# Optimization experiments

Hardware: AMD Instinct MI355X
Metric: run time of the kernel (lower is better)

The kernel has to match this reference:

```python
import jax, jax.numpy as jnp
import numpy as np

N_HIDDEN = 512

def _lstm_cell(x, h, c, W_ih, W_hh, b):
    # PyTorch LSTMCell: gates ordered i, f, g, o
    gates = x @ W_ih.T + h @ W_hh.T + b  # [B, 4H]
    i, f, g, o = jnp.split(gates, 4, axis=-1)
    i = jax.nn.sigmoid(i)
    f = jax.nn.sigmoid(f)
    g = jnp.tanh(g)
    o = jax.nn.sigmoid(o)
    c_new = f * c + i * g
    h_new = o * jnp.tanh(c_new)
    return h_new, c_new

def setup_inputs() -> dict:
    key = jax.random.key(0)
    ks = jax.random.split(key, 10)
    B, T, H = 256, 1024, N_HIDDEN
    s1 = 1.0 / np.sqrt(H)
    inp = {
        'x': jax.random.normal(ks[0], (B, T), dtype=jnp.float32),
        'W_ih1': jax.random.uniform(ks[1], (4 * H, 1), jnp.float32, -s1, s1),
        'W_hh1': jax.random.uniform(ks[2], (4 * H, H), jnp.float32, -s1, s1),
        'b1': jax.random.uniform(ks[3], (4 * H,), jnp.float32, -s1, s1),
        'W_ih2': jax.random.uniform(ks[4], (4 * H, H), jnp.float32, -s1, s1),
        'W_hh2': jax.random.uniform(ks[5], (4 * H, H), jnp.float32, -s1, s1),
        'b2': jax.random.uniform(ks[6], (4 * H,), jnp.float32, -s1, s1),
        'W_lin': jax.random.uniform(ks[7], (1, H), jnp.float32, -s1, s1),
        'b_lin': jax.random.uniform(ks[8], (1,), jnp.float32, -s1, s1),
    }
    return inp

def reference(x, W_ih1, W_hh1, b1, W_ih2, W_hh2, b2, W_lin, b_lin):
    B, T = x.shape
    H = W_hh1.shape[1]
    zeros = jnp.zeros((B, H), dtype=x.dtype)
    init = (zeros, zeros, zeros, zeros)
    xs = x.T[:, :, None]  # [T, B, 1]

    def step(carry, x_t):
        h1, c1, h2, c2 = carry
        h1, c1 = _lstm_cell(x_t, h1, c1, W_ih1, W_hh1, b1)
        h2, c2 = _lstm_cell(h1, h2, c2, W_ih2, W_hh2, b2)
        out = h2 @ W_lin.T + b_lin  # [B, 1]
        return (h1, c1, h2, c2), out

    _, outs = jax.lax.scan(step, init, xs)  # outs: [T, B, 1]
    return outs[:, :, 0].T  # [B, T]
```

## Files before the change

### kernel.cpp

```cpp
#include <hip/hip_runtime.h>
#include <math.h>

#define BB   256
#define TT   1024
#define HH   512
#define NWG  256
#define NTHR 512
#define SLOT (HH*BB)
#define NSLOT 8
#define PADX 20

typedef _Float16 f16;
typedef _Float16 f16x8 __attribute__((ext_vector_type(8)));
typedef float    f32x4 __attribute__((ext_vector_type(4)));
typedef unsigned int u32;
typedef u32 u32x2 __attribute__((ext_vector_type(2)));
typedef u32 u32x4 __attribute__((ext_vector_type(4)));
typedef unsigned short u16;
typedef unsigned char u8;

__device__ __forceinline__ f32x4 mf(f16x8 a, f16x8 b, f32x4 c){
  return __builtin_amdgcn_mfma_f32_16x16x32_f16(a, b, c, 0, 0, 0);
}

__device__ __forceinline__ float fast_sigmoid(float v){
  float e = __expf(-v);
  return __builtin_amdgcn_rcpf(1.0f + e);
}
__device__ __forceinline__ float fast_tanh(float v){
  float a = fabsf(v);
  float e = __expf(-2.0f * a);
  float r = (1.0f - e) * __builtin_amdgcn_rcpf(1.0f + e);
  return copysignf(r, v);
}

__device__ __forceinline__ void split_h(float hv, u16& hb, u8& lb){
  const f16 hh = (f16)hv;
  const f16 lh = (f16)((hv - (float)hh) * 2048.0f);
  union {f16 f; u16 u;} ch, cl; ch.f = hh; cl.f = lh;
  hb = ch.u;
  lb = (u8)(((u32)cl.u + 0x80u) >> 8);
}
__device__ __forceinline__ float join_h(u16 hb, u8 lb){
  union {u16 u; f16 f;} h, l;
  h.u = hb; l.u = (u16)((u32)lb << 8);
  return (float)h.f + (float)l.f * (1.0f/2048.0f);
}
__device__ __forceinline__ void st_wt_u16(u16* p, u16 v){
  __hip_atomic_store(p, v, __ATOMIC_RELAXED, __HIP_MEMORY_SCOPE_AGENT);
}
__device__ __forceinline__ void st_wt_u8(u8* p, u8 v){
  __hip_atomic_store(p, v, __ATOMIC_RELAXED, __HIP_MEMORY_SCOPE_AGENT);
}
__device__ __forceinline__ void st_wt_f32(float* p, float v){
  __hip_atomic_store(p, v, __ATOMIC_RELAXED, __HIP_MEMORY_SCOPE_AGENT);
}

__device__ __forceinline__ void build2(u32x4 hd, u32x2 ld2, f16x8& fh, f16x8& fl){
  union {u32 u[4]; f16x8 f;} H, L;
  H.u[0]=hd[0]; H.u[1]=hd[1]; H.u[2]=hd[2]; H.u[3]=hd[3];
  L.u[0] = __builtin_amdgcn_perm(ld2[0], 0u, 0x05010400u);
  L.u[1] = __builtin_amdgcn_perm(ld2[0], 0u, 0x07010600u);
  L.u[2] = __builtin_amdgcn_perm(ld2[1], 0u, 0x05010400u);
  L.u[3] = __builtin_amdgcn_perm(ld2[1], 0u, 0x07010600u);
  fh = H.f; fl = L.f;
}

struct St { u32x4 h1h4; u32x2 h1l2; u32x4 h2h4; u32x2 h2l2; };

__device__ __forceinline__ void gridbar_g(unsigned* barb, unsigned ph){
  __syncthreads();
  if (threadIdx.x == 0){
    __builtin_amdgcn_fence(__ATOMIC_RELEASE, "agent");
    const unsigned g = blockIdx.x & 31u;
    unsigned old = __hip_atomic_fetch_add(&barb[g*16], 1u, __ATOMIC_RELAXED, __HIP_MEMORY_SCOPE_AGENT);
    if (old + 1u == 8u*ph){
      unsigned om = __hip_atomic_fetch_add(&barb[512], 1u, __ATOMIC_RELAXED, __HIP_MEMORY_SCOPE_AGENT);
      if (om + 1u == 32u*ph){
        #pragma unroll
        for (int r = 0; r < 32; ++r)
          __hip_atomic_store(&barb[544 + r*16], ph, __ATOMIC_RELAXED, __HIP_MEMORY_SCOPE_AGENT);
      }
    }
    while (__hip_atomic_load(&barb[544 + g*16], __ATOMIC_RELAXED, __HIP_MEMORY_SCOPE_AGENT) < ph){
      __builtin_amdgcn_s_sleep(2);
    }
    __builtin_amdgcn_fence(__ATOMIC_ACQUIRE, "agent");
  }
  __syncthreads();
}

__global__ __launch_bounds__(NTHR, 2) void lstm_mfma(
    const float* __restrict__ x,      const float* __restrict__ W_ih1,
    const float* __restrict__ W_hh1,  const float* __restrict__ b1,
    const float* __restrict__ W_ih2,  const float* __restrict__ W_hh2,
    const float* __restrict__ b2,     const float* __restrict__ W_lin,
    const float* __restrict__ b_lin,  float* __restrict__ out,
    char* __restrict__ wsb)
{
  __shared__ f16x8 A2hi[2048], A2lo[2048], A1hi[1024], A1lo[1024];
  __shared__ float xch[8][16*PADX];
  __shared__ float wlin_s[512];
  __shared__ float outpart[2][8];

  unsigned* bar = (unsigned*)wsb;
  float* xT = (float*)(wsb + 16384);
  u16* h1h = (u16*)(wsb + 16384 + 1048576);
  u8*  h1l = (u8*) ((char*)h1h + 2*NSLOT*SLOT);
  u16* h2h = (u16*)((char*)h1l + NSLOT*SLOT);
  u8*  h2l = (u8*) ((char*)h2h + 2*NSLOT*SLOT);

  const int w   = blockIdx.x,  tid = threadIdx.x;
  const int l   = tid & 63,    wv  = tid >> 6;
  const int quad = l >> 4,     lc  = l & 15;
  const int p = w >> 1, cb = w & 1;
  const int j0 = 4*p;
  const int bcol = cb*128 + wv*16 + lc;
  const int jq = j0 + quad;
  const int b_out = cb*128 + p;
  unsigned* dbar = bar + cb*1024;
  unsigned* gbar = bar + 2048;
  const unsigned grp = (unsigned)(p >> 3);
  const int qrot = p & 3;
  const int hoff = (p>>1)*2048 + bcol*8 + (p&1)*4 + quad;

  {
    const int g_ = lc >> 2, jj_ = lc & 3;
    const int wrow = g_*HH + j0 + jj_;
    const float* rowI  = W_ih2 + (size_t)wrow*HH;
    const float* rowH2 = W_hh2 + (size_t)wrow*HH;
    const float* rowH1 = W_hh1 + (size_t)wrow*HH;
    for (int c = wv; c < 32; c += 8){
      const int kb = c*32 + quad*8;
      union {f16x8 v; f16 e[8];} hi8, lo8;
      #pragma unroll
      for (int i = 0; i < 8; ++i){
        const int k = kb + i;
        const float wval = (k < HH) ? rowI[k] : rowH2[k - HH];
        const f16 h_ = (f16)wval;
        hi8.e[i] = h_;
        lo8.e[i] = (f16)((wval - (float)h_) * 2048.0f);
      }
      A2hi[c*64 + l] = hi8.v;
      A2lo[c*64 + l] = lo8.v;
    }
    for (int c = wv; c < 16; c += 8){
      const int kb = c*32 + quad*8;
      union {f16x8 v; f16 e[8];} hi8, lo8;
      #pragma unroll
      for (int i = 0; i < 8; ++i){
        const float wval = rowH1[kb + i];
        const f16 h_ = (f16)wval;
        hi8.e[i] = h_;
        lo8.e[i] = (f16)((wval - (float)h_) * 2048.0f);
      }
      A1hi[c*64 + l] = hi8.v;
      A1lo[c*64 + l] = lo8.v;
    }
  }
  float wih1r[4], b1r[4], b2r[4];
  #pragma unroll
  for (int g = 0; g < 4; ++g){
    wih1r[g] = W_ih1[g*HH + jq];
    b1r[g]   = b1[g*HH + jq];
    b2r[g]   = b2[g*HH + jq];
  }
  const float blin = b_lin[0];
  wlin_s[tid] = W_lin[tid];

  {
    const int gid = w*NTHR + tid;
    #pragma unroll
    for (int i2 = 0; i2 < 2; ++i2){
      const int idx = gid + i2*131072;
      const int bb2 = idx >> 10, tt2 = idx & (TT-1);
      xT[(size_t)tt2*BB + bb2] = x[idx];
    }
  }
  {
    const int idx = w*NTHR + tid;
    st_wt_u16(&h2h[(NSLOT-1)*SLOT + idx], (u16)0);
    st_wt_u8 (&h2l[(NSLOT-1)*SLOT + idx], (u8)0);
  }

  gridbar_g(gbar, 1);

  float c1, c2 = 0.0f;
  {
    const float xv0 = xT[bcol];
    const float gi = fast_sigmoid(fmaf(xv0, wih1r[0], b1r[0]));
    const float gg = fast_tanh   (fmaf(xv0, wih1r[2], b1r[2]));
    const float go = fast_sigmoid(fmaf(xv0, wih1r[3], b1r[3]));
    c1 = gi * gg;
    const float hv = go * fast_tanh(c1);
    u16 hb; u8 lb; split_h(hv, hb, lb);
    st_wt_u16(&h1h[hoff], hb);
    st_wt_u8 (&h1l[hoff], lb);
  }
  gridbar_g(gbar, 2);

  auto poll_mask = [&](unsigned need) -> unsigned {
    unsigned cv = __hip_atomic_load(&dbar[(l & 15) * 16], __ATOMIC_RELAXED, __HIP_MEMORY_SCOPE_AGENT);
    return (unsigned)__ballot(cv >= need) & 0xFFFFu;
  };

  unsigned got = 0xFFFFu;

  for (int t = 0; t < TT; ++t){
    const int sR1 = ( t            & (NSLOT-1))*SLOT;
    const int sR2 = ((t+NSLOT-1)   & (NSLOT-1))*SLOT;
    const int sW1 = ((t+1)         & (NSLOT-1))*SLOT;
    const int sW2 = ( t            & (NSLOT-1))*SLOT;
    const unsigned need = 8u * (unsigned)t;

    f32x4 aA2 = {0,0,0,0}, aB2 = {0,0,0,0}, aA1 = {0,0,0,0}, aB1 = {0,0,0,0};
    const u16* q1h = h1h + sR1 + quad*2048 + bcol*8;
    const u8*  q1l = h1l + sR1 + quad*2048 + bcol*8;
    const u16* q2h = h2h + sR2 + quad*2048 + bcol*8;
    const u8*  q2l = h2l + sR2 + quad*2048 + bcol*8;

    auto waitq = [&](int qq){
      const unsigned qm = 0xFu << (4*qq);
      while ((got & qm) != qm){
        __builtin_amdgcn_s_sleep(1);
        got |= poll_mask(need);
      }
      asm volatile("" ::: "memory");
    };
    auto ldc = [&](int c) -> St {
      St s;
      s.h1h4 = *(const u32x4*)(q1h + c*8192);
      s.h1l2 = *(const u32x2*)(q1l + c*8192);
      s.h2h4 = *(const u32x4*)(q2h + c*8192);
      s.h2l2 = *(const u32x2*)(q2l + c*8192);
      return s;
    };
    auto cmp = [&](const St& s, int c){
      f16x8 bh, bl;
      build2(s.h1h4, s.h1l2, bh, bl);
      const f16x8 a2h = A2hi[c*64 + l];
      const f16x8 a2l = A2lo[c*64 + l];
      const f16x8 a1h = A1hi[c*64 + l];
      const f16x8 a1l = A1lo[c*64 + l];
      aA2 = mf(a2h, bh, aA2);
      aB2 = mf(a2h, bl, aB2);
      aB2 = mf(a2l, bh, aB2);
      aA1 = mf(a1h, bh, aA1);
      aB1 = mf(a1h, bl, aB1);
      aB1 = mf(a1l, bh, aB1);
      f16x8 ch, cl2;
      build2(s.h2h4, s.h2l2, ch, cl2);
      const f16x8 d2h = A2hi[(c+16)*64 + l];
      const f16x8 d2l = A2lo[(c+16)*64 + l];
      aA2 = mf(d2h, ch, aA2);
      aB2 = mf(d2h, cl2, aB2);
      aB2 = mf(d2l, ch, aB2);
    };

    const int cq0 = 4*qrot;
    const int cq1 = 4*((qrot+1)&3);
    const int cq2 = 4*((qrot+2)&3);
    const int cq3 = 4*((qrot+3)&3);
    St SA0,SA1,SA2,SA3, SB0,SB1,SB2,SB3;
    waitq(cq0 >> 2);
    SA0=ldc(cq0+0); SA1=ldc(cq0+1); SA2=ldc(cq0+2); SA3=ldc(cq0+3);
    waitq(cq1 >> 2);
    SB0=ldc(cq1+0); SB1=ldc(cq1+1); SB2=ldc(cq1+2); SB3=ldc(cq1+3);
    cmp(SA0,cq0+0); cmp(SA1,cq0+1); cmp(SA2,cq0+2); cmp(SA3,cq0+3);
    waitq(cq2 >> 2);
    SA0=ldc(cq2+0); SA1=ldc(cq2+1); SA2=ldc(cq2+2); SA3=ldc(cq2+3);
    cmp(SB0,cq1+0); cmp(SB1,cq1+1); cmp(SB2,cq1+2); cmp(SB3,cq1+3);
    waitq(cq3 >> 2);
    SB0=ldc(cq3+0); SB1=ldc(cq3+1); SB2=ldc(cq3+2); SB3=ldc(cq3+3);
    cmp(SA0,cq2+0); cmp(SA1,cq2+1); cmp(SA2,cq2+2); cmp(SA3,cq2+3);
    cmp(SB0,cq3+0); cmp(SB1,cq3+1); cmp(SB2,cq3+2); cmp(SB3,cq3+3);

    const int oidx = sR2 + (tid>>3)*2048 + b_out*8 + (tid&7);
    float opart = join_h(h2h[oidx], h2l[oidx]) * wlin_s[tid];

    float* xw = &xch[wv][0];
    {
      f32x4 pre;
      #pragma unroll
      for (int i = 0; i < 4; ++i) pre[i] = fmaf(aB2[i], 1.0f/2048.0f, aA2[i]);
      *(f32x4*)&xw[lc*PADX + quad*4] = pre;
      __threadfence_block();
      const float g0 = xw[lc*PADX + 0*4 + quad];
      const float g1 = xw[lc*PADX + 1*4 + quad];
      const float g2 = xw[lc*PADX + 2*4 + quad];
      const float g3 = xw[lc*PADX + 3*4 + quad];
      const float gi = fast_sigmoid(g0 + b2r[0]);
      const float gf = fast_sigmoid(g1 + b2r[1]);
      const float gg = fast_tanh   (g2 + b2r[2]);
      const float go = fast_sigmoid(g3 + b2r[3]);
      c2 = fmaf(gf, c2, gi*gg);
      const float hv = go * fast_tanh(c2);
      u16 hb; u8 lb; split_h(hv, hb, lb);
      st_wt_u16(&h2h[sW2 + hoff], hb);
      st_wt_u8 (&h2l[sW2 + hoff], lb);
    }
    {
      f32x4 pre;
      #pragma unroll
      for (int i = 0; i < 4; ++i) pre[i] = fmaf(aB1[i], 1.0f/2048.0f, aA1[i]);
      __threadfence_block();
      *(f32x4*)&xw[lc*PADX + quad*4] = pre;
      __threadfence_block();
      const float g0 = xw[lc*PADX + 0*4 + quad];
      const float g1 = xw[lc*PADX + 1*4 + quad];
      const float g2 = xw[lc*PADX + 2*4 + quad];
      const float g3 = xw[lc*PADX + 3*4 + quad];
      const int tx = (t+1 < TT) ? (t+1) : (TT-1);
      const float xv = xT[(size_t)tx*BB + bcol];
      const float gi = fast_sigmoid(g0 + fmaf(xv, wih1r[0], b1r[0]));
      const float gf = fast_sigmoid(g1 + fmaf(xv, wih1r[1], b1r[1]));
      const float gg = fast_tanh   (g2 + fmaf(xv, wih1r[2], b1r[2]));
      const float go = fast_sigmoid(g3 + fmaf(xv, wih1r[3], b1r[3]));
      c1 = fmaf(gf, c1, gi*gg);
      const float hv = go * fast_tanh(c1);
      u16 hb; u8 lb; split_h(hv, hb, lb);
      st_wt_u16(&h1h[sW1 + hoff], hb);
      st_wt_u8 (&h1l[sW1 + hoff], lb);
    }
    #pragma unroll
    for (int off = 32; off > 0; off >>= 1) opart += __shfl_down(opart, off, 64);
    if (l == 0) outpart[t & 1][wv] = opart;

    __syncthreads();
    if (tid == 0){
      __builtin_amdgcn_fence(__ATOMIC_RELEASE, "workgroup");
      __hip_atomic_fetch_add(&dbar[grp*16], 1u, __ATOMIC_RELAXED, __HIP_MEMORY_SCOPE_AGENT);
      if (t % 7 == 6){
        __builtin_amdgcn_fence(__ATOMIC_ACQUIRE, "agent");
      }
      if (t > 0){
        float s = blin;
        #pragma unroll
        for (int q2i = 0; q2i < 8; ++q2i) s += outpart[t & 1][q2i];
        st_wt_f32(&out[(size_t)b_out*TT + (t-1)], s);
      }
    }
    got = poll_mask(8u * (unsigned)(t+1));
    __syncthreads();
  }

  {
    const unsigned needT = 8u * (unsigned)TT;
    while (got != 0xFFFFu){
      __builtin_amdgcn_s_sleep(1);
      got |= poll_mask(needT);
    }
    asm volatile("" ::: "memory");

    const int oidx = ((TT-1)&(NSLOT-1))*SLOT + (tid>>3)*2048 + b_out*8 + (tid&7);
    float opart = join_h(h2h[oidx], h2l[oidx]) * wlin_s[tid];
    #pragma unroll
    for (int off = 32; off > 0; off >>= 1) opart += __shfl_down(opart, off, 64);
    if (l == 0) outpart[0][wv] = opart;
    __syncthreads();
    if (tid == 0){
      float s = blin;
      #pragma unroll
      for (int q2i = 0; q2i < 8; ++q2i) s += outpart[0][q2i];
      st_wt_f32(&out[(size_t)b_out*TT + (TT-1)], s);
    }
  }
}

extern "C" void kernel_launch(void* const* d_in, const int* in_sizes, int n_in,
                              void* d_out, int out_size, void* d_ws, size_t ws_size,
                              hipStream_t stream) {
  const float* x     = (const float*)d_in[0];
  const float* W_ih1 = (const float*)d_in[1];
  const float* W_hh1 = (const float*)d_in[2];
  const float* b1    = (const float*)d_in[3];
  const float* W_ih2 = (const float*)d_in[4];
  const float* W_hh2 = (const float*)d_in[5];
  const float* b2    = (const float*)d_in[6];
  const float* W_lin = (const float*)d_in[7];
  const float* b_lin = (const float*)d_in[8];
  float* out = (float*)d_out;
  char* wsb  = (char*)d_ws;

  hipMemsetAsync(d_ws, 0, 16384, stream);

  hipLaunchKernelGGL(lstm_mfma, dim3(NWG), dim3(NTHR), 0, stream,
                     x, W_ih1, W_hh1, b1, W_ih2, W_hh2, b2, W_lin, b_lin, out, wsb);
}
```

Measured before the change: 10.73 ms.

## Split per-step sync into separate h1 and h2 barriers to overlap layers

Each timestep now runs in two phases. First the kernel computes the h1-dependent products and the layer-1 update, then signals a separate h1 counter. Only after that does it wait on h2 chunks for the recurrent layer-2 term. Separate dbar counters, polled with a 32-bit ballot, let layer-1 progress be published earlier so other workgroups can start the next step sooner. The cost is an extra __syncthreads and atomic per step, plus more polling.

```diff
diff --git a/kernel.cpp b/kernel.cpp
--- a/kernel.cpp
+++ b/kernel.cpp
@@ -66,7 +66,7 @@
   fh = H.f; fl = L.f;
 }
 
-struct St { u32x4 h1h4; u32x2 h1l2; u32x4 h2h4; u32x2 h2l2; };
+struct St1 { u32x4 h4; u32x2 l2; };
 
 __device__ __forceinline__ void gridbar_g(unsigned* barb, unsigned ph){
   __syncthreads();
@@ -199,12 +199,14 @@
   }
   gridbar_g(gbar, 2);
 
-  auto poll_mask = [&](unsigned need) -> unsigned {
-    unsigned cv = __hip_atomic_load(&dbar[(l & 15) * 16], __ATOMIC_RELAXED, __HIP_MEMORY_SCOPE_AGENT);
-    return (unsigned)__ballot(cv >= need) & 0xFFFFu;
+  auto poll2 = [&](unsigned need) -> unsigned {
+    const int li = l & 31;
+    const unsigned off = (unsigned)((li & 15) * 16) + ((li & 16) ? 576u : 0u);
+    unsigned cv = __hip_atomic_load(&dbar[off], __ATOMIC_RELAXED, __HIP_MEMORY_SCOPE_AGENT);
+    return (unsigned)__ballot(cv >= need);
   };
 
-  unsigned got = 0xFFFFu;
+  unsigned got = 0xFFFFFFFFu;
 
   for (int t = 0; t < TT; ++t){
     const int sR1 = ( t            & (NSLOT-1))*SLOT;
@@ -219,25 +221,23 @@
     const u16* q2h = h2h + sR2 + quad*2048 + bcol*8;
     const u8*  q2l = h2l + sR2 + quad*2048 + bcol*8;
 
-    auto waitq = [&](int qq){
-      const unsigned qm = 0xFu << (4*qq);
+    auto waitq = [&](int qq, int base){
+      const unsigned qm = 0xFu << (base + 4*qq);
       while ((got & qm) != qm){
         __builtin_amdgcn_s_sleep(1);
-        got |= poll_mask(need);
+        got |= poll2(need);
       }
       asm volatile("" ::: "memory");
     };
-    auto ldc = [&](int c) -> St {
-      St s;
-      s.h1h4 = *(const u32x4*)(q1h + c*8192);
-      s.h1l2 = *(const u32x2*)(q1l + c*8192);
-      s.h2h4 = *(const u32x4*)(q2h + c*8192);
-      s.h2l2 = *(const u32x2*)(q2l + c*8192);
-      return s;
+    auto ldc1 = [&](int c) -> St1 {
+      St1 s; s.h4 = *(const u32x4*)(q1h + c*8192); s.l2 = *(const u32x2*)(q1l + c*8192); return s;
     };
-    auto cmp = [&](const St& s, int c){
+    auto ldc2 = [&](int c) -> St1 {
+      St1 s; s.h4 = *(const u32x4*)(q2h + c*8192); s.l2 = *(const u32x2*)(q2l + c*8192); return s;
+    };
+    auto cmp1 = [&](const St1& s, int c){
       f16x8 bh, bl;
-      build2(s.h1h4, s.h1l2, bh, bl);
+      build2(s.h4, s.l2, bh, bl);
       const f16x8 a2h = A2hi[c*64 + l];
       const f16x8 a2l = A2lo[c*64 + l];
       const f16x8 a1h = A1hi[c*64 + l];
@@ -248,8 +248,10 @@
       aA1 = mf(a1h, bh, aA1);
       aB1 = mf(a1h, bl, aB1);
       aB1 = mf(a1l, bh, aB1);
+    };
+    auto cmp2 = [&](const St1& s, int c){
       f16x8 ch, cl2;
-      build2(s.h2h4, s.h2l2, ch, cl2);
+      build2(s.h4, s.l2, ch, cl2);
       const f16x8 d2h = A2hi[(c+16)*64 + l];
       const f16x8 d2l = A2lo[(c+16)*64 + l];
       aA2 = mf(d2h, ch, aA2);
@@ -261,44 +263,24 @@
     const int cq1 = 4*((qrot+1)&3);
     const int cq2 = 4*((qrot+2)&3);
     const int cq3 = 4*((qrot+3)&3);
-    St SA0,SA1,SA2,SA3, SB0,SB1,SB2,SB3;
-    waitq(cq0 >> 2);
-    SA0=ldc(cq0+0); SA1=ldc(cq0+1); SA2=ldc(cq0+2); SA3=ldc(cq0+3);
-    waitq(cq1 >> 2);
-    SB0=ldc(cq1+0); SB1=ldc(cq1+1); SB2=ldc(cq1+2); SB3=ldc(cq1+3);
-    cmp(SA0,cq0+0); cmp(SA1,cq0+1); cmp(SA2,cq0+2); cmp(SA3,cq0+3);
-    waitq(cq2 >> 2);
-    SA0=ldc(cq2+0); SA1=ldc(cq2+1); SA2=ldc(cq2+2); SA3=ldc(cq2+3);
-    cmp(SB0,cq1+0); cmp(SB1,cq1+1); cmp(SB2,cq1+2); cmp(SB3,cq1+3);
-    waitq(cq3 >> 2);
-    SB0=ldc(cq3+0); SB1=ldc(cq3+1); SB2=ldc(cq3+2); SB3=ldc(cq3+3);
-    cmp(SA0,cq2+0); cmp(SA1,cq2+1); cmp(SA2,cq2+2); cmp(SA3,cq2+3);
-    cmp(SB0,cq3+0); cmp(SB1,cq3+1); cmp(SB2,cq3+2); cmp(SB3,cq3+3);
-
-    const int oidx = sR2 + (tid>>3)*2048 + b_out*8 + (tid&7);
-    float opart = join_h(h2h[oidx], h2l[oidx]) * wlin_s[tid];
+
+    {
+      St1 SA0,SA1,SA2,SA3, SB0,SB1,SB2,SB3;
+      waitq(cq0 >> 2, 16);
+      SA0=ldc1(cq0+0); SA1=ldc1(cq0+1); SA2=ldc1(cq0+2); SA3=ldc1(cq0+3);
+      waitq(cq1 >> 2, 16);
+      SB0=ldc1(cq1+0); SB1=ldc1(cq1+1); SB2=ldc1(cq1+2); SB3=ldc1(cq1+3);
+      cmp1(SA0,cq0+0); cmp1(SA1,cq0+1); cmp1(SA2,cq0+2); cmp1(SA3,cq0+3);
+      waitq(cq2 >> 2, 16);
+      SA0=ldc1(cq2+0); SA1=ldc1(cq2+1); SA2=ldc1(cq2+2); SA3=ldc1(cq2+3);
+      cmp1(SB0,cq1+0); cmp1(SB1,cq1+1); cmp1(SB2,cq1+2); cmp1(SB3,cq1+3);
+      waitq(cq3 >> 2, 16);
+      SB0=ldc1(cq3+0); SB1=ldc1(cq3+1); SB2=ldc1(cq3+2); SB3=ldc1(cq3+3);
+      cmp1(SA0,cq2+0); cmp1(SA1,cq2+1); cmp1(SA2,cq2+2); cmp1(SA3,cq2+3);
+      cmp1(SB0,cq3+0); cmp1(SB1,cq3+1); cmp1(SB2,cq3+2); cmp1(SB3,cq3+3);
+    }
 
     float* xw = &xch[wv][0];
-    {
-      f32x4 pre;
-      #pragma unroll
-      for (int i = 0; i < 4; ++i) pre[i] = fmaf(aB2[i], 1.0f/2048.0f, aA2[i]);
-      *(f32x4*)&xw[lc*PADX + quad*4] = pre;
-      __threadfence_block();
-      const float g0 = xw[lc*PADX + 0*4 + quad];
-      const float g1 = xw[lc*PADX + 1*4 + quad];
-      const float g2 = xw[lc*PADX + 2*4 + quad];
-      const float g3 = xw[lc*PADX + 3*4 + quad];
-      const float gi = fast_sigmoid(g0 + b2r[0]);
-      const float gf = fast_sigmoid(g1 + b2r[1]);
-      const float gg = fast_tanh   (g2 + b2r[2]);
-      const float go = fast_sigmoid(g3 + b2r[3]);
-      c2 = fmaf(gf, c2, gi*gg);
-      const float hv = go * fast_tanh(c2);
-      u16 hb; u8 lb; split_h(hv, hb, lb);
-      st_wt_u16(&h2h[sW2 + hoff], hb);
-      st_wt_u8 (&h2l[sW2 + hoff], lb);
-    }
     {
       f32x4 pre;
       #pragma unroll
@@ -322,6 +304,55 @@
       st_wt_u16(&h1h[sW1 + hoff], hb);
       st_wt_u8 (&h1l[sW1 + hoff], lb);
     }
+    __syncthreads();
+    if (tid == 0){
+      __builtin_amdgcn_fence(__ATOMIC_RELEASE, "workgroup");
+      __hip_atomic_fetch_add(&dbar[576 + grp*16], 1u, __ATOMIC_RELAXED, __HIP_MEMORY_SCOPE_AGENT);
+    }
+
+    u16 ohb; u8 olb;
+    {
+      St1 SA0,SA1,SA2,SA3, SB0,SB1,SB2,SB3;
+      waitq(cq0 >> 2, 0);
+      SA0=ldc2(cq0+0); SA1=ldc2(cq0+1); SA2=ldc2(cq0+2); SA3=ldc2(cq0+3);
+      waitq(cq1 >> 2, 0);
+      SB0=ldc2(cq1+0); SB1=ldc2(cq1+1); SB2=ldc2(cq1+2); SB3=ldc2(cq1+3);
+      cmp2(SA0,cq0+0); cmp2(SA1,cq0+1); cmp2(SA2,cq0+2); cmp2(SA3,cq0+3);
+      waitq(cq2 >> 2, 0);
+      SA0=ldc2(cq2+0); SA1=ldc2(cq2+1); SA2=ldc2(cq2+2); SA3=ldc2(cq2+3);
+      cmp2(SB0,cq1+0); cmp2(SB1,cq1+1); cmp2(SB2,cq1+2); cmp2(SB3,cq1+3);
+      waitq(cq3 >> 2, 0);
+      SB0=ldc2(cq3+0); SB1=ldc2(cq3+1); SB2=ldc2(cq3+2); SB3=ldc2(cq3+3);
+      const int oidx = sR2 + (tid>>3)*2048 + b_out*8 + (tid&7);
+      ohb = h2h[oidx];
+      olb = h2l[oidx];
+      cmp2(SA0,cq2+0); cmp2(SA1,cq2+1); cmp2(SA2,cq2+2); cmp2(SA3,cq2+3);
+      cmp2(SB0,cq3+0); cmp2(SB1,cq3+1); cmp2(SB2,cq3+2); cmp2(SB3,cq3+3);
+    }
+
+    float opart = join_h(ohb, olb) * wlin_s[tid];
+
+    {
+      f32x4 pre;
+      #pragma unroll
+      for (int i = 0; i < 4; ++i) pre[i] = fmaf(aB2[i], 1.0f/2048.0f, aA2[i]);
+      __threadfence_block();
+      *(f32x4*)&xw[lc*PADX + quad*4] = pre;
+      __threadfence_block();
+      const float g0 = xw[lc*PADX + 0*4 + quad];
+      const float g1 = xw[lc*PADX + 1*4 + quad];
+      const float g2 = xw[lc*PADX + 2*4 + quad];
+      const float g3 = xw[lc*PADX + 3*4 + quad];
+      const float gi = fast_sigmoid(g0 + b2r[0]);
+      const float gf = fast_sigmoid(g1 + b2r[1]);
+      const float gg = fast_tanh   (g2 + b2r[2]);
+      const float go = fast_sigmoid(g3 + b2r[3]);
+      c2 = fmaf(gf, c2, gi*gg);
+      const float hv = go * fast_tanh(c2);
+      u16 hb; u8 lb; split_h(hv, hb, lb);
+      st_wt_u16(&h2h[sW2 + hoff], hb);
+      st_wt_u8 (&h2l[sW2 + hoff], lb);
+    }
     #pragma unroll
     for (int off = 32; off > 0; off >>= 1) opart += __shfl_down(opart, off, 64);
     if (l == 0) outpart[t & 1][wv] = opart;
@@ -340,15 +371,15 @@
         st_wt_f32(&out[(size_t)b_out*TT + (t-1)], s);
       }
     }
-    got = poll_mask(8u * (unsigned)(t+1));
+    got = poll2(8u * (unsigned)(t+1));
     __syncthreads();
   }
 
   {
     const unsigned needT = 8u * (unsigned)TT;
-    while (got != 0xFFFFu){
+    while ((got & 0xFFFFu) != 0xFFFFu){
       __builtin_amdgcn_s_sleep(1);
-      got |= poll_mask(needT);
+      got |= poll2(needT);
     }
     asm volatile("" ::: "memory");
 
```

New measurement: 13.03 ms. 1.21x slower.
